# Optimization experiments

Measured on AMD Instinct MI355X. Metric: run time of the kernel, lower is better.

Reference implementation:

```python
import jax, jax.numpy as jnp
import numpy as np

N_NODES = 50000


def gcn_conv(x, W, b, src, dst, n_nodes):
    """GCNConv (PyG defaults): h = D^{-1/2}(A+I)D^{-1/2} (x @ W) + b, edge weights = 1.
    Self loops handled analytically (self-loop norm = 1/deg_i) to avoid growing edge arrays."""
    h = x @ W  # [N, out]
    # degree including self loop, computed on destination (col) per PyG gcn_norm
    deg = jax.ops.segment_sum(jnp.ones(src.shape[0], h.dtype), dst, num_segments=n_nodes) + 1.0
    dinv = jax.lax.rsqrt(deg)  # deg >= 1 so no clamping needed
    norm = dinv[src] * dinv[dst]  # [E]
    agg = jax.ops.segment_sum(h[src] * norm[:, None], dst, num_segments=n_nodes)
    agg = agg + h * (dinv * dinv)[:, None]  # self-loop contribution
    return agg + b


def setup_inputs() -> dict:
    key = jax.random.key(0)
    ks = jax.random.split(key, 6)
    n, e, d_in, d_hid = N_NODES, 800000, 128, 16
    x = jax.random.normal(ks[0], (n, d_in), dtype=jnp.float32)
    edge_index = jax.random.randint(ks[1], (2, e), 0, n, dtype=jnp.int64)
    W1 = jax.random.normal(ks[2], (d_in, d_hid), dtype=jnp.float32) * (1.0 / np.sqrt(d_in))
    b1 = jnp.zeros((d_hid,), jnp.float32)
    W2 = jax.random.normal(ks[3], (d_hid, d_in), dtype=jnp.float32) * (1.0 / np.sqrt(d_hid))
    b2 = jnp.zeros((d_in,), jnp.float32)
    return {"x": x, "edge_index": edge_index, "W1": W1, "b1": b1, "W2": W2, "b2": b2}


def reference(x, edge_index, W1, b1, W2, b2):
    src, dst = edge_index[0], edge_index[1]
    z = gcn_conv(x, W1, b1, src, dst, N_NODES)          # encoder: 128 -> 16
    recon = gcn_conv(z, W2, b2, src, dst, N_NODES)      # decoder: 16 -> 128
    return recon
```

## Files before the change

### kernel.cpp

```cpp
#include <hip/hip_runtime.h>


#define N_NODES 50000
#define N_EDGES 800000
#define D_IN    128
#define D_H     16
#define K_BUCK  512
#define NPB2    98
#define BSHIFT  11
#define BCAP    (1 << BSHIFT)
#define PA_BLKS 500
#define PA_CHUNK 1600
#define GC_PAD  16

__global__ __launch_bounds__(256) void k1_fused(
        const int* __restrict__ src, const int* __restrict__ dst,
        const float* __restrict__ x, const float* __restrict__ W1,
        int* __restrict__ gcur, float* __restrict__ h1, int* __restrict__ arr) {
    __shared__ float w1s[D_IN * D_H];
    __shared__ int hist[K_BUCK];
    __shared__ int cur[K_BUCK];
    int bid = blockIdx.x;
    int tid = threadIdx.x;

    if (bid < PA_BLKS) {
        int e0 = bid * PA_CHUNK;
        for (int b = tid; b < K_BUCK; b += 256) hist[b] = 0;
        __syncthreads();
        for (int i = tid; i < PA_CHUNK; i += 256) {
            int d = dst[e0 + i];
            atomicAdd(&hist[d / NPB2], 1);
        }
        __syncthreads();
        for (int b = tid; b < K_BUCK; b += 256)
            cur[b] = (b << BSHIFT) + atomicAdd(&gcur[b * GC_PAD], hist[b]);
        __syncthreads();
        for (int i = tid; i < PA_CHUNK; i += 256) {
            int d = dst[e0 + i];
            int s = src[e0 + i];
            int b = d / NPB2;
            int pos = atomicAdd(&cur[b], 1);
            if (pos < ((b + 1) << BSHIFT))
                arr[pos] = (s << 7) | (d - b * NPB2);
        }
    } else {
        for (int i = tid; i < D_IN * D_H; i += 256) w1s[i] = W1[i];
        __syncthreads();
        int idx = (bid - PA_BLKS) * 256 + tid;
        int row = idx >> 4;
        int col = idx & 15;
        const float4* xr = (const float4*)(x + row * D_IN);
        float acc = 0.0f;
        #pragma unroll
        for (int k4 = 0; k4 < D_IN / 4; ++k4) {
            float4 v = xr[k4];
            acc += v.x * w1s[(k4 * 4 + 0) * D_H + col];
            acc += v.y * w1s[(k4 * 4 + 1) * D_H + col];
            acc += v.z * w1s[(k4 * 4 + 2) * D_H + col];
            acc += v.w * w1s[(k4 * 4 + 3) * D_H + col];
        }
        h1[idx] = acc;
    }
}

__global__ __launch_bounds__(256) void k2_build_csr(
        const int* __restrict__ arr, const int* __restrict__ gcur,
        float* __restrict__ h1, float* __restrict__ dinv,
        int* __restrict__ csr, int2* __restrict__ meta) {
    __shared__ int cnt[NPB2];
    __shared__ int pref[NPB2];
    __shared__ int cur[NPB2];
    __shared__ float sdi[NPB2];
    int k = blockIdx.x, tid = threadIdx.x;
    for (int i = tid; i < NPB2; i += 256) cnt[i] = 0;
    __syncthreads();
    int count = min(gcur[k * GC_PAD], BCAP);
    int base = k << BSHIFT;
    for (int i = tid; i < count; i += 256) atomicAdd(&cnt[arr[base + i] & 127], 1);
    __syncthreads();
    if (tid == 0) {
        int run = 0;
        for (int l = 0; l < NPB2; ++l) { pref[l] = run; run += cnt[l]; }
    }
    __syncthreads();
    int n0 = k * NPB2;
    int ncnt = min(NPB2, N_NODES - n0);
    for (int l = tid; l < ncnt; l += 256) {
        cur[l] = pref[l];
        meta[n0 + l] = make_int2(base + pref[l], cnt[l]);
        float di = rsqrtf((float)cnt[l] + 1.0f);
        sdi[l] = di;
        dinv[n0 + l] = di;
    }
    __syncthreads();
    for (int g = tid; g < ncnt * 4; g += 256) {
        int l = g >> 2;
        float di = sdi[l];
        float4* p = (float4*)(h1 + (n0 + l) * D_H);
        float4 v = p[g & 3];
        v.x *= di; v.y *= di; v.z *= di; v.w *= di;
        p[g & 3] = v;
    }
    for (int i = tid; i < count; i += 256) {
        int p = arr[base + i];
        int l = p & 127;
        int pos = atomicAdd(&cur[l], 1);
        csr[base + pos] = p >> 7;
    }
}

__global__ __launch_bounds__(256) void k3_agg_enc(
        const float4* __restrict__ h1s4, const int* __restrict__ csr,
        const int2* __restrict__ meta, const float* __restrict__ dinv,
        const float* __restrict__ b1, float4* __restrict__ zs4) {
    int tid = threadIdx.x;
    int q = tid & 3;
    int n = blockIdx.x * 64 + (tid >> 2);
    if (n >= N_NODES) return;
    int qb = tid & 60;
    int2 m = meta[n];
    int e = m.x, end = m.x + m.y;
    float4 acc = {0.0f, 0.0f, 0.0f, 0.0f};
    for (; e < end; e += 4) {
        int myidx = 0;
        if (e + q < end) myidx = csr[e + q];
        #pragma unroll
        for (int j = 0; j < 4; ++j) {
            int idx = __shfl(myidx, qb + j, 64);
            if (e + j < end) {
                float4 v = h1s4[idx * 4 + q];
                acc.x += v.x; acc.y += v.y; acc.z += v.z; acc.w += v.w;
            }
        }
    }
    float di = dinv[n];
    float4 hv = h1s4[n * 4 + q];
    float4 bv = ((const float4*)b1)[q];
    float4 z;
    z.x = di * (di * (acc.x + hv.x) + bv.x);
    z.y = di * (di * (acc.y + hv.y) + bv.y);
    z.z = di * (di * (acc.z + hv.z) + bv.z);
    z.w = di * (di * (acc.w + hv.w) + bv.w);
    zs4[n * 4 + q] = z;
}

__global__ __launch_bounds__(256) void k4_agg_dec_out(
        const float4* __restrict__ zs4, const int* __restrict__ csr,
        const int2* __restrict__ meta, const float* __restrict__ dinv,
        const float* __restrict__ W2, const float* __restrict__ b2,
        float* __restrict__ out) {
    __shared__ __align__(16) float agL[64 * D_H];
    __shared__ __align__(16) float w2s[D_H * D_IN];
    int tid = threadIdx.x;
    for (int i = tid; i < D_H * D_IN; i += 256) w2s[i] = W2[i];
    int q = tid & 3;
    int nloc = tid >> 2;
    int n = blockIdx.x * 64 + nloc;
    int qb = tid & 60;
    if (n < N_NODES) {
        int2 m = meta[n];
        int e = m.x, end = m.x + m.y;
        float4 acc = {0.0f, 0.0f, 0.0f, 0.0f};
        for (; e < end; e += 4) {
            int myidx = 0;
            if (e + q < end) myidx = csr[e + q];
            #pragma unroll
            for (int j = 0; j < 4; ++j) {
                int idx = __shfl(myidx, qb + j, 64);
                if (e + j < end) {
                    float4 v = zs4[idx * 4 + q];
                    acc.x += v.x; acc.y += v.y; acc.z += v.z; acc.w += v.w;
                }
            }
        }
        float di = dinv[n];
        float4 zv = zs4[n * 4 + q];
        float4 a;
        a.x = di * (acc.x + zv.x);
        a.y = di * (acc.y + zv.y);
        a.z = di * (acc.z + zv.z);
        a.w = di * (acc.w + zv.w);
        ((float4*)agL)[nloc * 4 + q] = a;
    }
    __syncthreads();
    int total = min(64, N_NODES - (int)blockIdx.x * 64);
    if (nloc < total) {
        const float* arow = &agL[nloc * D_H];
        const float4* w2s4 = (const float4*)w2s;
        float4 o[8];
        #pragma unroll
        for (int u = 0; u < 8; ++u) o[u] = ((const float4*)b2)[q * 8 + u];
        #pragma unroll
        for (int c = 0; c < D_H; ++c) {
            float ac = arow[c];
            #pragma unroll
            for (int u = 0; u < 8; ++u) {
                float4 w = w2s4[c * (D_IN / 4) + q * 8 + u];
                o[u].x += ac * w.x; o[u].y += ac * w.y;
                o[u].z += ac * w.z; o[u].w += ac * w.w;
            }
        }
        float4* orow = (float4*)(out + n * D_IN);
        #pragma unroll
        for (int u = 0; u < 8; ++u) orow[q * 8 + u] = o[u];
    }
}

extern "C" void kernel_launch(void* const* d_in, const int* in_sizes, int n_in,
                              void* d_out, int out_size, void* d_ws, size_t ws_size,
                              hipStream_t stream) {
    const float* x  = (const float*)d_in[0];
    const int*   ei = (const int*)d_in[1];
    const float* W1 = (const float*)d_in[2];
    const float* b1 = (const float*)d_in[3];
    const float* W2 = (const float*)d_in[4];
    const float* b2 = (const float*)d_in[5];
    float* out = (float*)d_out;

    const int* src = ei;
    const int* dst = ei + N_EDGES;

    char* base = (char*)d_ws;
    int*    gcur = (int*)base;                 base += K_BUCK * GC_PAD * 4;
    float*  dinv = (float*)base;               base += N_NODES * 4;
    float*  h1   = (float*)base;               base += N_NODES * D_H * 4;
    float*  zs   = (float*)base;               base += N_NODES * D_H * 4;
    int2*   meta = (int2*)base;                base += N_NODES * 8;
    int*    arr  = (int*)base;                 base += K_BUCK * BCAP * 4;
    int*    csr  = (int*)base;                 base += K_BUCK * BCAP * 4;

    hipMemsetAsync(gcur, 0, K_BUCK * GC_PAD * sizeof(int), stream);

    k1_fused<<<PA_BLKS + (N_NODES * D_H / 256), 256, 0, stream>>>(src, dst, x, W1, gcur, h1, arr);
    k2_build_csr<<<K_BUCK, 256, 0, stream>>>(arr, gcur, h1, dinv, csr, meta);
    k3_agg_enc<<<(N_NODES + 63) / 64, 256, 0, stream>>>((const float4*)h1, csr, meta, dinv, b1, (float4*)zs);
    k4_agg_dec_out<<<(N_NODES + 63) / 64, 256, 0, stream>>>((const float4*)zs, csr, meta, dinv, W2, b2, out);
}
```

Before: 167.1 us.

## Vectorize edge partition loads, row-per-thread encoder GEMM, and remap decoder output GEMM

After: 162.0 us. 1.03x faster.

```diff
diff --git a/kernel.cpp b/kernel.cpp
--- a/kernel.cpp
+++ b/kernel.cpp
@@ -12,12 +12,14 @@
 #define PA_BLKS 500
 #define PA_CHUNK 1600
 #define GC_PAD  16
+#define G_BLKS  196
+#define K4_NPB  128
 
 __global__ __launch_bounds__(256) void k1_fused(
         const int* __restrict__ src, const int* __restrict__ dst,
         const float* __restrict__ x, const float* __restrict__ W1,
         int* __restrict__ gcur, float* __restrict__ h1, int* __restrict__ arr) {
-    __shared__ float w1s[D_IN * D_H];
+    __shared__ __align__(16) float w1s[D_IN * D_H];
     __shared__ int hist[K_BUCK];
     __shared__ int cur[K_BUCK];
     int bid = blockIdx.x;
@@ -27,39 +29,55 @@
         int e0 = bid * PA_CHUNK;
         for (int b = tid; b < K_BUCK; b += 256) hist[b] = 0;
         __syncthreads();
-        for (int i = tid; i < PA_CHUNK; i += 256) {
-            int d = dst[e0 + i];
-            atomicAdd(&hist[d / NPB2], 1);
+        const int4* d4p = (const int4*)(dst + e0);
+        const int4* s4p = (const int4*)(src + e0);
+        for (int i = tid; i < PA_CHUNK / 4; i += 256) {
+            int4 d = d4p[i];
+            atomicAdd(&hist[d.x / NPB2], 1);
+            atomicAdd(&hist[d.y / NPB2], 1);
+            atomicAdd(&hist[d.z / NPB2], 1);
+            atomicAdd(&hist[d.w / NPB2], 1);
         }
         __syncthreads();
         for (int b = tid; b < K_BUCK; b += 256)
             cur[b] = (b << BSHIFT) + atomicAdd(&gcur[b * GC_PAD], hist[b]);
         __syncthreads();
-        for (int i = tid; i < PA_CHUNK; i += 256) {
-            int d = dst[e0 + i];
-            int s = src[e0 + i];
-            int b = d / NPB2;
-            int pos = atomicAdd(&cur[b], 1);
-            if (pos < ((b + 1) << BSHIFT))
-                arr[pos] = (s << 7) | (d - b * NPB2);
+        for (int i = tid; i < PA_CHUNK / 4; i += 256) {
+            int4 d = d4p[i];
+            int4 s = s4p[i];
+            int b0 = d.x / NPB2, b1 = d.y / NPB2, b2 = d.z / NPB2, b3 = d.w / NPB2;
+            int p0 = atomicAdd(&cur[b0], 1);
+            int p1 = atomicAdd(&cur[b1], 1);
+            int p2 = atomicAdd(&cur[b2], 1);
+            int p3 = atomicAdd(&cur[b3], 1);
+            if (p0 < ((b0 + 1) << BSHIFT)) arr[p0] = (s.x << 7) | (d.x - b0 * NPB2);
+            if (p1 < ((b1 + 1) << BSHIFT)) arr[p1] = (s.y << 7) | (d.y - b1 * NPB2);
+            if (p2 < ((b2 + 1) << BSHIFT)) arr[p2] = (s.z << 7) | (d.z - b2 * NPB2);
+            if (p3 < ((b3 + 1) << BSHIFT)) arr[p3] = (s.w << 7) | (d.w - b3 * NPB2);
         }
     } else {
         for (int i = tid; i < D_IN * D_H; i += 256) w1s[i] = W1[i];
         __syncthreads();
-        int idx = (bid - PA_BLKS) * 256 + tid;
-        int row = idx >> 4;
-        int col = idx & 15;
+        int row = (bid - PA_BLKS) * 256 + tid;
+        if (row >= N_NODES) return;
         const float4* xr = (const float4*)(x + row * D_IN);
-        float acc = 0.0f;
-        #pragma unroll
+        const float4* w4 = (const float4*)w1s;
+        float4 a0 = {0, 0, 0, 0}, a1 = a0, a2 = a0, a3 = a0;
         for (int k4 = 0; k4 < D_IN / 4; ++k4) {
-            float4 v = xr[k4];
-            acc += v.x * w1s[(k4 * 4 + 0) * D_H + col];
-            acc += v.y * w1s[(k4 * 4 + 1) * D_H + col];
-            acc += v.z * w1s[(k4 * 4 + 2) * D_H + col];
-            acc += v.w * w1s[(k4 * 4 + 3) * D_H + col];
-        }
-        h1[idx] = acc;
+            float4 xv = xr[k4];
+            #pragma unroll
+            for (int j = 0; j < 4; ++j) {
+                float xk = (j == 0) ? xv.x : (j == 1) ? xv.y : (j == 2) ? xv.z : xv.w;
+                const float4* wr = w4 + (k4 * 4 + j) * 4;
+                float4 w0 = wr[0], w1v = wr[1], w2v = wr[2], w3v = wr[3];
+                a0.x += xk * w0.x;  a0.y += xk * w0.y;  a0.z += xk * w0.z;  a0.w += xk * w0.w;
+                a1.x += xk * w1v.x; a1.y += xk * w1v.y; a1.z += xk * w1v.z; a1.w += xk * w1v.w;
+                a2.x += xk * w2v.x; a2.y += xk * w2v.y; a2.z += xk * w2v.z; a2.w += xk * w2v.w;
+                a3.x += xk * w3v.x; a3.y += xk * w3v.y; a3.z += xk * w3v.z; a3.w += xk * w3v.w;
+            }
+        }
+        float4* hr = (float4*)(h1 + row * D_H);
+        hr[0] = a0; hr[1] = a1; hr[2] = a2; hr[3] = a3;
     }
 }
 
@@ -144,18 +162,19 @@
     zs4[n * 4 + q] = z;
 }
 
-__global__ __launch_bounds__(256) void k4_agg_dec_out(
+__global__ __launch_bounds__(512) void k4_agg_dec_out(
         const float4* __restrict__ zs4, const int* __restrict__ csr,
         const int2* __restrict__ meta, const float* __restrict__ dinv,
         const float* __restrict__ W2, const float* __restrict__ b2,
         float* __restrict__ out) {
-    __shared__ __align__(16) float agL[64 * D_H];
+    __shared__ float agL[K4_NPB * 17];
     __shared__ __align__(16) float w2s[D_H * D_IN];
     int tid = threadIdx.x;
-    for (int i = tid; i < D_H * D_IN; i += 256) w2s[i] = W2[i];
+    for (int i = tid; i < D_H * D_IN; i += 512) w2s[i] = W2[i];
     int q = tid & 3;
     int nloc = tid >> 2;
-    int n = blockIdx.x * 64 + nloc;
+    int n0 = blockIdx.x * K4_NPB;
+    int n = n0 + nloc;
     int qb = tid & 60;
     if (n < N_NODES) {
         int2 m = meta[n];
@@ -175,34 +194,34 @@
         }
         float di = dinv[n];
         float4 zv = zs4[n * 4 + q];
-        float4 a;
-        a.x = di * (acc.x + zv.x);
-        a.y = di * (acc.y + zv.y);
-        a.z = di * (acc.z + zv.z);
-        a.w = di * (acc.w + zv.w);
-        ((float4*)agL)[nloc * 4 + q] = a;
-    }
-    __syncthreads();
-    int total = min(64, N_NODES - (int)blockIdx.x * 64);
-    if (nloc < total) {
-        const float* arow = &agL[nloc * D_H];
-        const float4* w2s4 = (const float4*)w2s;
+        agL[nloc * 17 + q * 4 + 0] = di * (acc.x + zv.x);
+        agL[nloc * 17 + q * 4 + 1] = di * (acc.y + zv.y);
+        agL[nloc * 17 + q * 4 + 2] = di * (acc.z + zv.z);
+        agL[nloc * 17 + q * 4 + 3] = di * (acc.w + zv.w);
+    }
+    __syncthreads();
+    int quarter = tid >> 7;
+    int ne = tid & 127;
+    if (n0 + ne < N_NODES) {
+        const float* arow = &agL[ne * 17];
         float4 o[8];
-        #pragma unroll
-        for (int u = 0; u < 8; ++u) o[u] = ((const float4*)b2)[q * 8 + u];
+        const float4* b2q = (const float4*)(b2 + quarter * 32);
+        #pragma unroll
+        for (int u = 0; u < 8; ++u) o[u] = b2q[u];
         #pragma unroll
         for (int c = 0; c < D_H; ++c) {
             float ac = arow[c];
+            const float4* wr = (const float4*)(w2s + c * D_IN + quarter * 32);
             #pragma unroll
             for (int u = 0; u < 8; ++u) {
-                float4 w = w2s4[c * (D_IN / 4) + q * 8 + u];
+                float4 w = wr[u];
                 o[u].x += ac * w.x; o[u].y += ac * w.y;
                 o[u].z += ac * w.z; o[u].w += ac * w.w;
             }
         }
-        float4* orow = (float4*)(out + n * D_IN);
-        #pragma unroll
-        for (int u = 0; u < 8; ++u) orow[q * 8 + u] = o[u];
+        float4* orow = (float4*)(out + (n0 + ne) * D_IN + quarter * 32);
+        #pragma unroll
+        for (int u = 0; u < 8; ++u) orow[u] = o[u];
     }
 }
 
@@ -231,8 +250,8 @@
 
     hipMemsetAsync(gcur, 0, K_BUCK * GC_PAD * sizeof(int), stream);
 
-    k1_fused<<<PA_BLKS + (N_NODES * D_H / 256), 256, 0, stream>>>(src, dst, x, W1, gcur, h1, arr);
+    k1_fused<<<PA_BLKS + G_BLKS, 256, 0, stream>>>(src, dst, x, W1, gcur, h1, arr);
     k2_build_csr<<<K_BUCK, 256, 0, stream>>>(arr, gcur, h1, dinv, csr, meta);
     k3_agg_enc<<<(N_NODES + 63) / 64, 256, 0, stream>>>((const float4*)h1, csr, meta, dinv, b1, (float4*)zs);
-    k4_agg_dec_out<<<(N_NODES + 63) / 64, 256, 0, stream>>>((const float4*)zs, csr, meta, dinv, W2, b2, out);
-}
+    k4_agg_dec_out<<<(N_NODES + K4_NPB - 1) / K4_NPB, 512, 0, stream>>>((const float4*)zs, csr, meta, dinv, W2, b2, out);
+}
```
